# Performance work log

Hardware: AMD Instinct MI355X
Metric: run time of the kernel (lower is better)

## Reference

```python
import jax, jax.numpy as jnp
import numpy as np

N_NODES = 50000
N_EDGES = 800000
D = 96  # d_node = d_edge = hidden = out


def setup_inputs() -> dict:
    key = jax.random.key(0)
    ks = jax.random.split(key, 12)
    s = 1.0 / np.sqrt(D)
    inp = {
        "x": jax.random.normal(ks[0], (N_NODES, D), dtype=jnp.float32),
        "edge_index": jax.random.randint(ks[1], (2, N_EDGES), 0, N_NODES, dtype=jnp.int64),
        "edge_attr": jax.random.normal(ks[2], (N_EDGES, D), dtype=jnp.float32),
        # f_node params: MLP on concat(x, agg_edge_attr) -> [2D] -> D -> D
        "Wn1": jax.random.normal(ks[3], (2 * D, D), dtype=jnp.float32) * s,
        "bn1": jnp.zeros((D,), dtype=jnp.float32),
        "Wn2": jax.random.normal(ks[4], (D, D), dtype=jnp.float32) * s,
        "bn2": jnp.zeros((D,), dtype=jnp.float32),
        # f_edge params: MLP on concat(src, dst, edge_attr) -> [3D] -> D -> D
        "We1": jax.random.normal(ks[5], (3 * D, D), dtype=jnp.float32) * s,
        "be1": jnp.zeros((D,), dtype=jnp.float32),
        "We2": jax.random.normal(ks[6], (D, D), dtype=jnp.float32) * s,
        "be2": jnp.zeros((D,), dtype=jnp.float32),
    }
    return inp


def reference(x, edge_index, edge_attr, Wn1, bn1, Wn2, bn2, We1, be1, We2, be2):
    n_nodes = x.shape[0]
    # f_node: aggregate incoming edge features to destination nodes, then MLP
    agg = jax.ops.segment_sum(edge_attr, edge_index[1], num_segments=n_nodes)  # [N, D]
    hn = jax.nn.relu(jnp.concatenate([x, agg], axis=-1) @ Wn1 + bn1)
    h_v = hn @ Wn2 + bn2  # [N, D]
    # f_edge: gather src/dst node features (x[edge_index[0]], x[edge_index[1]]), then MLP
    src = x[edge_index[0]]  # [E, D]
    dst = x[edge_index[1]]  # [E, D]
    he = jax.nn.relu(jnp.concatenate([src, dst, edge_attr], axis=-1) @ We1 + be1)
    h_e = he @ We2 + be2  # [E, D]
    return (h_v, edge_index, h_e)
```

## Files before the change

### kernel.cpp

```cpp
#include <hip/hip_runtime.h>

#define N_NODES 50000
#define N_EDGES 800000
#define DIM 96

#define BM 64
#define BK 48
#define APAD 52
#define HPAD 100

#define SC_CNT 0
#define SC_OFF 50000
#define SC_CUR 100016
#define SC_BSUM 150016
#define SC_EIDX 150528
#define NBLK_SCAN 196

#define FMA4(C, A, W)        \
  C.x = fmaf(A, W.x, C.x);   \
  C.y = fmaf(A, W.y, C.y);   \
  C.z = fmaf(A, W.z, C.z);   \
  C.w = fmaf(A, W.w, C.w)

#define BIAS_RELU4(C, B)          \
  C.x = fmaxf(C.x + B.x, 0.0f);   \
  C.y = fmaxf(C.y + B.y, 0.0f);   \
  C.z = fmaxf(C.z + B.z, 0.0f);   \
  C.w = fmaxf(C.w + B.w, 0.0f)

#define BIAS4(C, B) \
  C.x += B.x;       \
  C.y += B.y;       \
  C.z += B.z;       \
  C.w += B.w

#define KSTEP(KK, A0, A1)                                                    \
  {                                                                          \
    const float4 w0 =                                                        \
        *reinterpret_cast<const float4*>(&Ws[(k + KK) * DIM + cbase + 0]);   \
    const float4 w1 =                                                        \
        *reinterpret_cast<const float4*>(&Ws[(k + KK) * DIM + cbase + 4]);   \
    const float4 w2 =                                                        \
        *reinterpret_cast<const float4*>(&Ws[(k + KK) * DIM + cbase + 8]);   \
    FMA4(c00, A0, w0);                                                       \
    FMA4(c01, A0, w1);                                                       \
    FMA4(c02, A0, w2);                                                       \
    FMA4(c10, A1, w0);                                                       \
    FMA4(c11, A1, w1);                                                       \
    FMA4(c12, A1, w2);                                                       \
  }

__global__ __launch_bounds__(256) void hist_kernel(const int* __restrict__ ei,
                                                   int* __restrict__ sc) {
  int e = blockIdx.x * 256 + threadIdx.x;
  if (e < N_EDGES) atomicAdd(&sc[SC_CNT + ei[N_EDGES + e]], 1);
}

__global__ __launch_bounds__(256) void scan1_kernel(int* __restrict__ sc) {
  __shared__ int s[256];
  int i = blockIdx.x * 256 + threadIdx.x;
  s[threadIdx.x] = (i < N_NODES) ? sc[SC_CNT + i] : 0;
  __syncthreads();
  for (int off = 128; off > 0; off >>= 1) {
    if (threadIdx.x < off) s[threadIdx.x] += s[threadIdx.x + off];
    __syncthreads();
  }
  if (threadIdx.x == 0) sc[SC_BSUM + blockIdx.x] = s[0];
}

__global__ __launch_bounds__(256) void scan2_kernel(int* __restrict__ sc) {
  __shared__ int s[2][256];
  const int t = threadIdx.x;
  const int v = (t < NBLK_SCAN) ? sc[SC_BSUM + t] : 0;
  int cur = 0;
  s[0][t] = v;
  __syncthreads();
  for (int off = 1; off < 256; off <<= 1) {
    int nv = s[cur][t];
    if (t >= off) nv += s[cur][t - off];
    s[cur ^ 1][t] = nv;
    cur ^= 1;
    __syncthreads();
  }
  if (t < NBLK_SCAN) sc[SC_BSUM + t] = s[cur][t] - v;
}

__global__ __launch_bounds__(256) void scan3_kernel(int* __restrict__ sc) {
  __shared__ int s[2][256];
  const int t = threadIdx.x;
  const int i = blockIdx.x * 256 + t;
  const int v = (i < N_NODES) ? sc[SC_CNT + i] : 0;
  int cur = 0;
  s[0][t] = v;
  __syncthreads();
  for (int off = 1; off < 256; off <<= 1) {
    int nv = s[cur][t];
    if (t >= off) nv += s[cur][t - off];
    s[cur ^ 1][t] = nv;
    cur ^= 1;
    __syncthreads();
  }
  if (i < N_NODES) {
    const int excl = sc[SC_BSUM + blockIdx.x] + s[cur][t] - v;
    sc[SC_OFF + i] = excl;
    sc[SC_CUR + i] = excl;
  }
  if (i == 0) sc[SC_OFF + N_NODES] = N_EDGES;
}

__global__ __launch_bounds__(256) void fill_kernel(const int* __restrict__ ei,
                                                   int* __restrict__ sc) {
  int e = blockIdx.x * 256 + threadIdx.x;
  if (e < N_EDGES) {
    const int d = ei[N_EDGES + e];
    const int pos = atomicAdd(&sc[SC_CUR + d], 1);
    sc[SC_EIDX + pos] = e;
  }
}

__global__ __launch_bounds__(192) void gather_kernel(
    const float* __restrict__ ea, const int* __restrict__ sc,
    float* __restrict__ agg) {
  const int t = threadIdx.x;
  const int ln = t / 24;
  const int q = t - ln * 24;
  const int n = blockIdx.x * 8 + ln;
  const int beg = sc[SC_OFF + n];
  const int end = sc[SC_OFF + n + 1];
  float4 acc = make_float4(0.f, 0.f, 0.f, 0.f);
  int e = (beg < end) ? sc[SC_EIDX + beg] : 0;
  for (int i = beg; i < end; ++i) {
    const int en = (i + 1 < end) ? sc[SC_EIDX + i + 1] : 0;
    const float4 v =
        *reinterpret_cast<const float4*>(ea + (size_t)e * DIM + q * 4);
    acc.x += v.x;
    acc.y += v.y;
    acc.z += v.z;
    acc.w += v.w;
    e = en;
  }
  *reinterpret_cast<float4*>(agg + (size_t)n * DIM + q * 4) = acc;
}

__global__ __launch_bounds__(256) void copy_ei_kernel(
    const int* __restrict__ ei, float* __restrict__ out) {
  int tid = blockIdx.x * 256 + threadIdx.x;
  if (tid < 2 * N_EDGES) out[tid] = (float)ei[tid];
}

__global__ __launch_bounds__(256, 3) void node_mlp_kernel(
    const float* __restrict__ x, const float* __restrict__ agg,
    const float* __restrict__ W1, const float* __restrict__ b1,
    const float* __restrict__ W2, const float* __restrict__ b2,
    float* __restrict__ out) {
  __shared__ float Ws[BK * DIM];
  __shared__ float AH[BM * HPAD];

  const int t = threadIdx.x;
  const int tx = t & 7;
  const int ty = t >> 3;
  const int r0 = ty * 2;
  const int n0 = blockIdx.x * BM;
  const int cbase = tx * 12;

  float4 c00 = make_float4(0.f, 0.f, 0.f, 0.f);
  float4 c01 = c00, c02 = c00, c10 = c00, c11 = c00, c12 = c00;

  for (int ch = 0; ch < 4; ++ch) {
    const int k0 = ch * BK;
    __syncthreads();
#pragma unroll
    for (int m = 0; m < 3; ++m) {
      const int idx = m * 256 + t;
      const int row = idx / 12;
      const int c4 = (idx - row * 12) * 4;
      const int col = k0 + c4;
      int n = n0 + row;
      n = (n < N_NODES) ? n : 0;
      const float* src = (col < DIM) ? x + (size_t)n * DIM + col
                                     : agg + (size_t)n * DIM + (col - DIM);
      *reinterpret_cast<float4*>(&AH[row * APAD + c4]) =
          *reinterpret_cast<const float4*>(src);
    }
#pragma unroll
    for (int m = 0; m < 5; ++m) {
      const int idx = m * 256 + t;
      if (idx < (BK * DIM) / 4) {
        const int wr = idx / 24;
        const int wc = (idx - wr * 24) * 4;
        *reinterpret_cast<float4*>(&Ws[wr * DIM + wc]) =
            *reinterpret_cast<const float4*>(W1 + (size_t)(k0 + wr) * DIM + wc);
      }
    }
    __syncthreads();
#pragma unroll
    for (int k = 0; k < BK; k += 4) {
      const float4 a0v =
          *reinterpret_cast<const float4*>(&AH[(r0 + 0) * APAD + k]);
      const float4 a1v =
          *reinterpret_cast<const float4*>(&AH[(r0 + 1) * APAD + k]);
      KSTEP(0, a0v.x, a1v.x);
      KSTEP(1, a0v.y, a1v.y);
      KSTEP(2, a0v.z, a1v.z);
      KSTEP(3, a0v.w, a1v.w);
    }
  }

  __syncthreads();

  {
    const float4 bb0 = *reinterpret_cast<const float4*>(b1 + cbase + 0);
    const float4 bb1 = *reinterpret_cast<const float4*>(b1 + cbase + 4);
    const float4 bb2 = *reinterpret_cast<const float4*>(b1 + cbase + 8);
    BIAS_RELU4(c00, bb0);
    BIAS_RELU4(c01, bb1);
    BIAS_RELU4(c02, bb2);
    BIAS_RELU4(c10, bb0);
    BIAS_RELU4(c11, bb1);
    BIAS_RELU4(c12, bb2);
    *reinterpret_cast<float4*>(&AH[(r0 + 0) * HPAD + cbase + 0]) = c00;
    *reinterpret_cast<float4*>(&AH[(r0 + 0) * HPAD + cbase + 4]) = c01;
    *reinterpret_cast<float4*>(&AH[(r0 + 0) * HPAD + cbase + 8]) = c02;
    *reinterpret_cast<float4*>(&AH[(r0 + 1) * HPAD + cbase + 0]) = c10;
    *reinterpret_cast<float4*>(&AH[(r0 + 1) * HPAD + cbase + 4]) = c11;
    *reinterpret_cast<float4*>(&AH[(r0 + 1) * HPAD + cbase + 8]) = c12;
  }

  c00 = make_float4(0.f, 0.f, 0.f, 0.f);
  c01 = c00;
  c02 = c00;
  c10 = c00;
  c11 = c00;
  c12 = c00;
  for (int ch = 0; ch < 2; ++ch) {
    const int k0 = ch * BK;
    __syncthreads();
#pragma unroll
    for (int m = 0; m < 5; ++m) {
      const int idx = m * 256 + t;
      if (idx < (BK * DIM) / 4) {
        const int wr = idx / 24;
        const int wc = (idx - wr * 24) * 4;
        *reinterpret_cast<float4*>(&Ws[wr * DIM + wc]) =
            *reinterpret_cast<const float4*>(W2 + (size_t)(k0 + wr) * DIM + wc);
      }
    }
    __syncthreads();
#pragma unroll
    for (int k = 0; k < BK; k += 4) {
      const float4 a0v =
          *reinterpret_cast<const float4*>(&AH[(r0 + 0) * HPAD + k0 + k]);
      const float4 a1v =
          *reinterpret_cast<const float4*>(&AH[(r0 + 1) * HPAD + k0 + k]);
      KSTEP(0, a0v.x, a1v.x);
      KSTEP(1, a0v.y, a1v.y);
      KSTEP(2, a0v.z, a1v.z);
      KSTEP(3, a0v.w, a1v.w);
    }
  }

  {
    const float4 bb0 = *reinterpret_cast<const float4*>(b2 + cbase + 0);
    const float4 bb1 = *reinterpret_cast<const float4*>(b2 + cbase + 4);
    const float4 bb2 = *reinterpret_cast<const float4*>(b2 + cbase + 8);
    BIAS4(c00, bb0);
    BIAS4(c01, bb1);
    BIAS4(c02, bb2);
    BIAS4(c10, bb0);
    BIAS4(c11, bb1);
    BIAS4(c12, bb2);
    const int n_r0 = n0 + r0;
    if (n_r0 < N_NODES) {
      float* o = out + (size_t)n_r0 * DIM + cbase;
      *reinterpret_cast<float4*>(o + 0) = c00;
      *reinterpret_cast<float4*>(o + 4) = c01;
      *reinterpret_cast<float4*>(o + 8) = c02;
    }
    if (n_r0 + 1 < N_NODES) {
      float* o = out + (size_t)(n_r0 + 1) * DIM + cbase;
      *reinterpret_cast<float4*>(o + 0) = c10;
      *reinterpret_cast<float4*>(o + 4) = c11;
      *reinterpret_cast<float4*>(o + 8) = c12;
    }
  }
}

__global__ __launch_bounds__(256, 3) void edge_mlp_kernel(
    const float* __restrict__ x, const int* __restrict__ ei,
    const float* __restrict__ ea, const float* __restrict__ W1,
    const float* __restrict__ b1, const float* __restrict__ W2,
    const float* __restrict__ b2, float* __restrict__ out) {
  __shared__ int s_src[BM];
  __shared__ int s_dst[BM];
  __shared__ float Ws[BK * DIM];
  __shared__ float AH[BM * HPAD];

  const int t = threadIdx.x;
  const int tx = t & 7;
  const int ty = t >> 3;
  const int r0 = ty * 2;
  const int e0 = blockIdx.x * BM;
  const int cbase = tx * 12;

  if (t < BM) {
    s_src[t] = ei[e0 + t];
    s_dst[t] = ei[N_EDGES + e0 + t];
  }

  float4 c00 = make_float4(0.f, 0.f, 0.f, 0.f);
  float4 c01 = c00, c02 = c00, c10 = c00, c11 = c00, c12 = c00;

  for (int ch = 0; ch < 6; ++ch) {
    const int k0 = ch * BK;
    __syncthreads();
#pragma unroll
    for (int m = 0; m < 3; ++m) {
      const int idx = m * 256 + t;
      const int row = idx / 12;
      const int c4 = (idx - row * 12) * 4;
      const int col = k0 + c4;
      const float* src;
      if (col < DIM)
        src = x + (size_t)s_src[row] * DIM + col;
      else if (col < 2 * DIM)
        src = x + (size_t)s_dst[row] * DIM + (col - DIM);
      else
        src = ea + (size_t)(e0 + row) * DIM + (col - 2 * DIM);
      *reinterpret_cast<float4*>(&AH[row * APAD + c4]) =
          *reinterpret_cast<const float4*>(src);
    }
#pragma unroll
    for (int m = 0; m < 5; ++m) {
      const int idx = m * 256 + t;
      if (idx < (BK * DIM) / 4) {
        const int wr = idx / 24;
        const int wc = (idx - wr * 24) * 4;
        *reinterpret_cast<float4*>(&Ws[wr * DIM + wc]) =
            *reinterpret_cast<const float4*>(W1 + (size_t)(k0 + wr) * DIM + wc);
      }
    }
    __syncthreads();
#pragma unroll
    for (int k = 0; k < BK; k += 4) {
      const float4 a0v =
          *reinterpret_cast<const float4*>(&AH[(r0 + 0) * APAD + k]);
      const float4 a1v =
          *reinterpret_cast<const float4*>(&AH[(r0 + 1) * APAD + k]);
      KSTEP(0, a0v.x, a1v.x);
      KSTEP(1, a0v.y, a1v.y);
      KSTEP(2, a0v.z, a1v.z);
      KSTEP(3, a0v.w, a1v.w);
    }
  }

  __syncthreads();

  {
    const float4 bb0 = *reinterpret_cast<const float4*>(b1 + cbase + 0);
    const float4 bb1 = *reinterpret_cast<const float4*>(b1 + cbase + 4);
    const float4 bb2 = *reinterpret_cast<const float4*>(b1 + cbase + 8);
    BIAS_RELU4(c00, bb0);
    BIAS_RELU4(c01, bb1);
    BIAS_RELU4(c02, bb2);
    BIAS_RELU4(c10, bb0);
    BIAS_RELU4(c11, bb1);
    BIAS_RELU4(c12, bb2);
    *reinterpret_cast<float4*>(&AH[(r0 + 0) * HPAD + cbase + 0]) = c00;
    *reinterpret_cast<float4*>(&AH[(r0 + 0) * HPAD + cbase + 4]) = c01;
    *reinterpret_cast<float4*>(&AH[(r0 + 0) * HPAD + cbase + 8]) = c02;
    *reinterpret_cast<float4*>(&AH[(r0 + 1) * HPAD + cbase + 0]) = c10;
    *reinterpret_cast<float4*>(&AH[(r0 + 1) * HPAD + cbase + 4]) = c11;
    *reinterpret_cast<float4*>(&AH[(r0 + 1) * HPAD + cbase + 8]) = c12;
  }

  c00 = make_float4(0.f, 0.f, 0.f, 0.f);
  c01 = c00;
  c02 = c00;
  c10 = c00;
  c11 = c00;
  c12 = c00;
  for (int ch = 0; ch < 2; ++ch) {
    const int k0 = ch * BK;
    __syncthreads();
#pragma unroll
    for (int m = 0; m < 5; ++m) {
      const int idx = m * 256 + t;
      if (idx < (BK * DIM) / 4) {
        const int wr = idx / 24;
        const int wc = (idx - wr * 24) * 4;
        *reinterpret_cast<float4*>(&Ws[wr * DIM + wc]) =
            *reinterpret_cast<const float4*>(W2 + (size_t)(k0 + wr) * DIM + wc);
      }
    }
    __syncthreads();
#pragma unroll
    for (int k = 0; k < BK; k += 4) {
      const float4 a0v =
          *reinterpret_cast<const float4*>(&AH[(r0 + 0) * HPAD + k0 + k]);
      const float4 a1v =
          *reinterpret_cast<const float4*>(&AH[(r0 + 1) * HPAD + k0 + k]);
      KSTEP(0, a0v.x, a1v.x);
      KSTEP(1, a0v.y, a1v.y);
      KSTEP(2, a0v.z, a1v.z);
      KSTEP(3, a0v.w, a1v.w);
    }
  }

  {
    const float4 bb0 = *reinterpret_cast<const float4*>(b2 + cbase + 0);
    const float4 bb1 = *reinterpret_cast<const float4*>(b2 + cbase + 4);
    const float4 bb2 = *reinterpret_cast<const float4*>(b2 + cbase + 8);
    BIAS4(c00, bb0);
    BIAS4(c01, bb1);
    BIAS4(c02, bb2);
    BIAS4(c10, bb0);
    BIAS4(c11, bb1);
    BIAS4(c12, bb2);
    float* o0 = out + (size_t)(e0 + r0) * DIM + cbase;
    float* o1 = out + (size_t)(e0 + r0 + 1) * DIM + cbase;
    *reinterpret_cast<float4*>(o0 + 0) = c00;
    *reinterpret_cast<float4*>(o0 + 4) = c01;
    *reinterpret_cast<float4*>(o0 + 8) = c02;
    *reinterpret_cast<float4*>(o1 + 0) = c10;
    *reinterpret_cast<float4*>(o1 + 4) = c11;
    *reinterpret_cast<float4*>(o1 + 8) = c12;
  }
}

extern "C" void kernel_launch(void* const* d_in, const int* in_sizes, int n_in,
                              void* d_out, int out_size, void* d_ws,
                              size_t ws_size, hipStream_t stream) {
  const float* x = (const float*)d_in[0];
  const int* ei = (const int*)d_in[1];
  const float* edge_attr = (const float*)d_in[2];
  const float* Wn1 = (const float*)d_in[3];
  const float* bn1 = (const float*)d_in[4];
  const float* Wn2 = (const float*)d_in[5];
  const float* bn2 = (const float*)d_in[6];
  const float* We1 = (const float*)d_in[7];
  const float* be1 = (const float*)d_in[8];
  const float* We2 = (const float*)d_in[9];
  const float* be2 = (const float*)d_in[10];

  float* out = (float*)d_out;
  float* agg = (float*)d_ws;

  float* out_hv = out;
  float* out_ei = out + (size_t)N_NODES * DIM;
  float* out_he = out + (size_t)N_NODES * DIM + 2 * (size_t)N_EDGES;

  int* sc = (int*)out_he;

  hipMemsetAsync(sc + SC_CNT, 0, N_NODES * sizeof(int), stream);
  hist_kernel<<<(N_EDGES + 255) / 256, 256, 0, stream>>>(ei, sc);
  scan1_kernel<<<NBLK_SCAN, 256, 0, stream>>>(sc);
  scan2_kernel<<<1, 256, 0, stream>>>(sc);
  scan3_kernel<<<NBLK_SCAN, 256, 0, stream>>>(sc);
  fill_kernel<<<(N_EDGES + 255) / 256, 256, 0, stream>>>(ei, sc);
  gather_kernel<<<N_NODES / 8, 192, 0, stream>>>(edge_attr, sc, agg);

  copy_ei_kernel<<<(2 * N_EDGES + 255) / 256, 256, 0, stream>>>(ei, out_ei);
  node_mlp_kernel<<<(N_NODES + BM - 1) / BM, 256, 0, stream>>>(
      x, agg, Wn1, bn1, Wn2, bn2, out_hv);
  edge_mlp_kernel<<<N_EDGES / BM, 256, 0, stream>>>(x, ei, edge_attr, We1, be1,
                                                    We2, be2, out_he);
}
```

Measured before the change: 1.649 ms.

## Double the MLP row tile and prefetch next K-chunk into registers

Both node and edge MLP kernels move from 64 to 128 rows per block, with each thread now computing 4 rows by 12 columns. This doubles register-level reuse of each weight float4 loaded from shared memory. A register-staged software pipeline is added that loads the next A/W chunk from global memory while the current chunk is computed. W2's first chunk is prefetched during the last layer-1 chunk. The cost is higher register pressure and occupancy lowered to 2 blocks per SM via launch bounds.

```diff
diff --git a/kernel.cpp b/kernel.cpp
--- a/kernel.cpp
+++ b/kernel.cpp
@@ -4,7 +4,7 @@
 #define N_EDGES 800000
 #define DIM 96
 
-#define BM 64
+#define BM 128
 #define BK 48
 #define APAD 52
 #define HPAD 100
@@ -34,7 +34,7 @@
   C.z += B.z;       \
   C.w += B.w
 
-#define KSTEP(KK, A0, A1)                                                    \
+#define KQ(KK, A0, A1, A2, A3)                                               \
   {                                                                          \
     const float4 w0 =                                                        \
         *reinterpret_cast<const float4*>(&Ws[(k + KK) * DIM + cbase + 0]);   \
@@ -42,13 +42,33 @@
         *reinterpret_cast<const float4*>(&Ws[(k + KK) * DIM + cbase + 4]);   \
     const float4 w2 =                                                        \
         *reinterpret_cast<const float4*>(&Ws[(k + KK) * DIM + cbase + 8]);   \
-    FMA4(c00, A0, w0);                                                       \
-    FMA4(c01, A0, w1);                                                       \
-    FMA4(c02, A0, w2);                                                       \
-    FMA4(c10, A1, w0);                                                       \
-    FMA4(c11, A1, w1);                                                       \
-    FMA4(c12, A1, w2);                                                       \
-  }
+    FMA4(c00, A0, w0); FMA4(c01, A0, w1); FMA4(c02, A0, w2);                 \
+    FMA4(c10, A1, w0); FMA4(c11, A1, w1); FMA4(c12, A1, w2);                 \
+    FMA4(c20, A2, w0); FMA4(c21, A2, w1); FMA4(c22, A2, w2);                 \
+    FMA4(c30, A3, w0); FMA4(c31, A3, w1); FMA4(c32, A3, w2);                 \
+  }
+
+#define COMPUTE_CHUNK(STRIDE, KOFF)                                          \
+  _Pragma("unroll") for (int k = 0; k < BK; k += 4) {                        \
+    const float4 av0 = *reinterpret_cast<const float4*>(                     \
+        &AH[(r0 + 0) * STRIDE + KOFF + k]);                                  \
+    const float4 av1 = *reinterpret_cast<const float4*>(                     \
+        &AH[(r0 + 1) * STRIDE + KOFF + k]);                                  \
+    const float4 av2 = *reinterpret_cast<const float4*>(                     \
+        &AH[(r0 + 2) * STRIDE + KOFF + k]);                                  \
+    const float4 av3 = *reinterpret_cast<const float4*>(                     \
+        &AH[(r0 + 3) * STRIDE + KOFF + k]);                                  \
+    KQ(0, av0.x, av1.x, av2.x, av3.x);                                       \
+    KQ(1, av0.y, av1.y, av2.y, av3.y);                                       \
+    KQ(2, av0.z, av1.z, av2.z, av3.z);                                       \
+    KQ(3, av0.w, av1.w, av2.w, av3.w);                                       \
+  }
+
+#define ZERO_ACC()                                          \
+  c00 = make_float4(0.f, 0.f, 0.f, 0.f);                    \
+  c01 = c00; c02 = c00; c10 = c00; c11 = c00; c12 = c00;    \
+  c20 = c00; c21 = c00; c22 = c00; c30 = c00; c31 = c00;    \
+  c32 = c00;
 
 __global__ __launch_bounds__(256) void hist_kernel(const int* __restrict__ ei,
                                                    int* __restrict__ sc) {
@@ -148,7 +168,7 @@
   if (tid < 2 * N_EDGES) out[tid] = (float)ei[tid];
 }
 
-__global__ __launch_bounds__(256, 3) void node_mlp_kernel(
+__global__ __launch_bounds__(256, 2) void node_mlp_kernel(
     const float* __restrict__ x, const float* __restrict__ agg,
     const float* __restrict__ W1, const float* __restrict__ b1,
     const float* __restrict__ W2, const float* __restrict__ b2,
@@ -159,133 +179,144 @@
   const int t = threadIdx.x;
   const int tx = t & 7;
   const int ty = t >> 3;
-  const int r0 = ty * 2;
+  const int r0 = ty * 4;
   const int n0 = blockIdx.x * BM;
   const int cbase = tx * 12;
 
-  float4 c00 = make_float4(0.f, 0.f, 0.f, 0.f);
-  float4 c01 = c00, c02 = c00, c10 = c00, c11 = c00, c12 = c00;
-
+  int arow[6], acol[6];
+#pragma unroll
+  for (int m = 0; m < 6; ++m) {
+    const int idx = m * 256 + t;
+    arow[m] = idx / 12;
+    acol[m] = (idx - arow[m] * 12) * 4;
+  }
+  int wr[5], wc[5];
+#pragma unroll
+  for (int m = 0; m < 5; ++m) {
+    const int idx = m * 256 + t;
+    wr[m] = idx / 24;
+    wc[m] = (idx - wr[m] * 24) * 4;
+  }
+
+  float4 ra[6], rw[5];
+
+  auto load_a = [&](int ch) {
+#pragma unroll
+    for (int m = 0; m < 6; ++m) {
+      const int col = ch * BK + acol[m];
+      int n = n0 + arow[m];
+      n = (n < N_NODES) ? n : 0;
+      const float* p = (col < DIM) ? x + (size_t)n * DIM + col
+                                   : agg + (size_t)n * DIM + (col - DIM);
+      ra[m] = *reinterpret_cast<const float4*>(p);
+    }
+  };
+  auto load_w = [&](const float* W, int ch) {
+#pragma unroll
+    for (int m = 0; m < 5; ++m)
+      if (m < 4 || t < 128)
+        rw[m] = *reinterpret_cast<const float4*>(
+            W + (size_t)(ch * BK + wr[m]) * DIM + wc[m]);
+  };
+  auto store_a = [&]() {
+#pragma unroll
+    for (int m = 0; m < 6; ++m)
+      *reinterpret_cast<float4*>(&AH[arow[m] * APAD + acol[m]]) = ra[m];
+  };
+  auto store_w = [&]() {
+#pragma unroll
+    for (int m = 0; m < 5; ++m)
+      if (m < 4 || t < 128)
+        *reinterpret_cast<float4*>(&Ws[wr[m] * DIM + wc[m]]) = rw[m];
+  };
+
+  float4 c00, c01, c02, c10, c11, c12, c20, c21, c22, c30, c31, c32;
+  ZERO_ACC();
+
+  load_a(0);
+  load_w(W1, 0);
   for (int ch = 0; ch < 4; ++ch) {
-    const int k0 = ch * BK;
-    __syncthreads();
-#pragma unroll
-    for (int m = 0; m < 3; ++m) {
-      const int idx = m * 256 + t;
-      const int row = idx / 12;
-      const int c4 = (idx - row * 12) * 4;
-      const int col = k0 + c4;
-      int n = n0 + row;
-      n = (n < N_NODES) ? n : 0;
-      const float* src = (col < DIM) ? x + (size_t)n * DIM + col
-                                     : agg + (size_t)n * DIM + (col - DIM);
-      *reinterpret_cast<float4*>(&AH[row * APAD + c4]) =
-          *reinterpret_cast<const float4*>(src);
-    }
-#pragma unroll
-    for (int m = 0; m < 5; ++m) {
-      const int idx = m * 256 + t;
-      if (idx < (BK * DIM) / 4) {
-        const int wr = idx / 24;
-        const int wc = (idx - wr * 24) * 4;
-        *reinterpret_cast<float4*>(&Ws[wr * DIM + wc]) =
-            *reinterpret_cast<const float4*>(W1 + (size_t)(k0 + wr) * DIM + wc);
-      }
-    }
-    __syncthreads();
-#pragma unroll
-    for (int k = 0; k < BK; k += 4) {
-      const float4 a0v =
-          *reinterpret_cast<const float4*>(&AH[(r0 + 0) * APAD + k]);
-      const float4 a1v =
-          *reinterpret_cast<const float4*>(&AH[(r0 + 1) * APAD + k]);
-      KSTEP(0, a0v.x, a1v.x);
-      KSTEP(1, a0v.y, a1v.y);
-      KSTEP(2, a0v.z, a1v.z);
-      KSTEP(3, a0v.w, a1v.w);
-    }
-  }
-
-  __syncthreads();
+    store_a();
+    store_w();
+    __syncthreads();
+    if (ch < 3) {
+      load_a(ch + 1);
+      load_w(W1, ch + 1);
+    } else {
+      load_w(W2, 0);
+    }
+    COMPUTE_CHUNK(APAD, 0);
+    __syncthreads();
+  }
 
   {
     const float4 bb0 = *reinterpret_cast<const float4*>(b1 + cbase + 0);
     const float4 bb1 = *reinterpret_cast<const float4*>(b1 + cbase + 4);
     const float4 bb2 = *reinterpret_cast<const float4*>(b1 + cbase + 8);
-    BIAS_RELU4(c00, bb0);
-    BIAS_RELU4(c01, bb1);
-    BIAS_RELU4(c02, bb2);
-    BIAS_RELU4(c10, bb0);
-    BIAS_RELU4(c11, bb1);
-    BIAS_RELU4(c12, bb2);
+    BIAS_RELU4(c00, bb0); BIAS_RELU4(c01, bb1); BIAS_RELU4(c02, bb2);
+    BIAS_RELU4(c10, bb0); BIAS_RELU4(c11, bb1); BIAS_RELU4(c12, bb2);
+    BIAS_RELU4(c20, bb0); BIAS_RELU4(c21, bb1); BIAS_RELU4(c22, bb2);
+    BIAS_RELU4(c30, bb0); BIAS_RELU4(c31, bb1); BIAS_RELU4(c32, bb2);
     *reinterpret_cast<float4*>(&AH[(r0 + 0) * HPAD + cbase + 0]) = c00;
     *reinterpret_cast<float4*>(&AH[(r0 + 0) * HPAD + cbase + 4]) = c01;
     *reinterpret_cast<float4*>(&AH[(r0 + 0) * HPAD + cbase + 8]) = c02;
     *reinterpret_cast<float4*>(&AH[(r0 + 1) * HPAD + cbase + 0]) = c10;
     *reinterpret_cast<float4*>(&AH[(r0 + 1) * HPAD + cbase + 4]) = c11;
     *reinterpret_cast<float4*>(&AH[(r0 + 1) * HPAD + cbase + 8]) = c12;
-  }
-
-  c00 = make_float4(0.f, 0.f, 0.f, 0.f);
-  c01 = c00;
-  c02 = c00;
-  c10 = c00;
-  c11 = c00;
-  c12 = c00;
-  for (int ch = 0; ch < 2; ++ch) {
-    const int k0 = ch * BK;
-    __syncthreads();
-#pragma unroll
-    for (int m = 0; m < 5; ++m) {
-      const int idx = m * 256 + t;
-      if (idx < (BK * DIM) / 4) {
-        const int wr = idx / 24;
-        const int wc = (idx - wr * 24) * 4;
-        *reinterpret_cast<float4*>(&Ws[wr * DIM + wc]) =
-            *reinterpret_cast<const float4*>(W2 + (size_t)(k0 + wr) * DIM + wc);
-      }
-    }
-    __syncthreads();
-#pragma unroll
-    for (int k = 0; k < BK; k += 4) {
-      const float4 a0v =
-          *reinterpret_cast<const float4*>(&AH[(r0 + 0) * HPAD + k0 + k]);
-      const float4 a1v =
-          *reinterpret_cast<const float4*>(&AH[(r0 + 1) * HPAD + k0 + k]);
-      KSTEP(0, a0v.x, a1v.x);
-      KSTEP(1, a0v.y, a1v.y);
-      KSTEP(2, a0v.z, a1v.z);
-      KSTEP(3, a0v.w, a1v.w);
-    }
-  }
+    *reinterpret_cast<float4*>(&AH[(r0 + 2) * HPAD + cbase + 0]) = c20;
+    *reinterpret_cast<float4*>(&AH[(r0 + 2) * HPAD + cbase + 4]) = c21;
+    *reinterpret_cast<float4*>(&AH[(r0 + 2) * HPAD + cbase + 8]) = c22;
+    *reinterpret_cast<float4*>(&AH[(r0 + 3) * HPAD + cbase + 0]) = c30;
+    *reinterpret_cast<float4*>(&AH[(r0 + 3) * HPAD + cbase + 4]) = c31;
+    *reinterpret_cast<float4*>(&AH[(r0 + 3) * HPAD + cbase + 8]) = c32;
+  }
+  store_w();
+  __syncthreads();
+
+  load_w(W2, 1);
+  ZERO_ACC();
+  COMPUTE_CHUNK(HPAD, 0);
+  __syncthreads();
+  store_w();
+  __syncthreads();
+  COMPUTE_CHUNK(HPAD, BK);
 
   {
     const float4 bb0 = *reinterpret_cast<const float4*>(b2 + cbase + 0);
     const float4 bb1 = *reinterpret_cast<const float4*>(b2 + cbase + 4);
     const float4 bb2 = *reinterpret_cast<const float4*>(b2 + cbase + 8);
-    BIAS4(c00, bb0);
-    BIAS4(c01, bb1);
-    BIAS4(c02, bb2);
-    BIAS4(c10, bb0);
-    BIAS4(c11, bb1);
-    BIAS4(c12, bb2);
-    const int n_r0 = n0 + r0;
-    if (n_r0 < N_NODES) {
-      float* o = out + (size_t)n_r0 * DIM + cbase;
+    BIAS4(c00, bb0); BIAS4(c01, bb1); BIAS4(c02, bb2);
+    BIAS4(c10, bb0); BIAS4(c11, bb1); BIAS4(c12, bb2);
+    BIAS4(c20, bb0); BIAS4(c21, bb1); BIAS4(c22, bb2);
+    BIAS4(c30, bb0); BIAS4(c31, bb1); BIAS4(c32, bb2);
+    if (n0 + r0 + 0 < N_NODES) {
+      float* o = out + (size_t)(n0 + r0 + 0) * DIM + cbase;
       *reinterpret_cast<float4*>(o + 0) = c00;
       *reinterpret_cast<float4*>(o + 4) = c01;
       *reinterpret_cast<float4*>(o + 8) = c02;
     }
-    if (n_r0 + 1 < N_NODES) {
-      float* o = out + (size_t)(n_r0 + 1) * DIM + cbase;
+    if (n0 + r0 + 1 < N_NODES) {
+      float* o = out + (size_t)(n0 + r0 + 1) * DIM + cbase;
       *reinterpret_cast<float4*>(o + 0) = c10;
       *reinterpret_cast<float4*>(o + 4) = c11;
       *reinterpret_cast<float4*>(o + 8) = c12;
     }
-  }
-}
-
-__global__ __launch_bounds__(256, 3) void edge_mlp_kernel(
+    if (n0 + r0 + 2 < N_NODES) {
+      float* o = out + (size_t)(n0 + r0 + 2) * DIM + cbase;
+      *reinterpret_cast<float4*>(o + 0) = c20;
+      *reinterpret_cast<float4*>(o + 4) = c21;
+      *reinterpret_cast<float4*>(o + 8) = c22;
+    }
+    if (n0 + r0 + 3 < N_NODES) {
+      float* o = out + (size_t)(n0 + r0 + 3) * DIM + cbase;
+      *reinterpret_cast<float4*>(o + 0) = c30;
+      *reinterpret_cast<float4*>(o + 4) = c31;
+      *reinterpret_cast<float4*>(o + 8) = c32;
+    }
+  }
+}
+
+__global__ __launch_bounds__(256, 2) void edge_mlp_kernel(
     const float* __restrict__ x, const int* __restrict__ ei,
     const float* __restrict__ ea, const float* __restrict__ W1,
     const float* __restrict__ b1, const float* __restrict__ W2,
@@ -298,132 +329,142 @@
   const int t = threadIdx.x;
   const int tx = t & 7;
   const int ty = t >> 3;
-  const int r0 = ty * 2;
+  const int r0 = ty * 4;
   const int e0 = blockIdx.x * BM;
   const int cbase = tx * 12;
 
-  if (t < BM) {
+  int arow[6], acol[6];
+#pragma unroll
+  for (int m = 0; m < 6; ++m) {
+    const int idx = m * 256 + t;
+    arow[m] = idx / 12;
+    acol[m] = (idx - arow[m] * 12) * 4;
+  }
+  int wr[5], wc[5];
+#pragma unroll
+  for (int m = 0; m < 5; ++m) {
+    const int idx = m * 256 + t;
+    wr[m] = idx / 24;
+    wc[m] = (idx - wr[m] * 24) * 4;
+  }
+
+  if (t < BM)
     s_src[t] = ei[e0 + t];
-    s_dst[t] = ei[N_EDGES + e0 + t];
-  }
-
-  float4 c00 = make_float4(0.f, 0.f, 0.f, 0.f);
-  float4 c01 = c00, c02 = c00, c10 = c00, c11 = c00, c12 = c00;
-
+  else
+    s_dst[t - BM] = ei[N_EDGES + e0 + (t - BM)];
+  __syncthreads();
+
+  float4 ra[6], rw[5];
+
+  auto load_a = [&](int ch) {
+#pragma unroll
+    for (int m = 0; m < 6; ++m) {
+      const int col = ch * BK + acol[m];
+      const int row = arow[m];
+      const float* p;
+      if (col < DIM)
+        p = x + (size_t)s_src[row] * DIM + col;
+      else if (col < 2 * DIM)
+        p = x + (size_t)s_dst[row] * DIM + (col - DIM);
+      else
+        p = ea + (size_t)(e0 + row) * DIM + (col - 2 * DIM);
+      ra[m] = *reinterpret_cast<const float4*>(p);
+    }
+  };
+  auto load_w = [&](const float* W, int ch) {
+#pragma unroll
+    for (int m = 0; m < 5; ++m)
+      if (m < 4 || t < 128)
+        rw[m] = *reinterpret_cast<const float4*>(
+            W + (size_t)(ch * BK + wr[m]) * DIM + wc[m]);
+  };
+  auto store_a = [&]() {
+#pragma unroll
+    for (int m = 0; m < 6; ++m)
+      *reinterpret_cast<float4*>(&AH[arow[m] * APAD + acol[m]]) = ra[m];
+  };
+  auto store_w = [&]() {
+#pragma unroll
+    for (int m = 0; m < 5; ++m)
+      if (m < 4 || t < 128)
+        *reinterpret_cast<float4*>(&Ws[wr[m] * DIM + wc[m]]) = rw[m];
+  };
+
+  float4 c00, c01, c02, c10, c11, c12, c20, c21, c22, c30, c31, c32;
+  ZERO_ACC();
+
+  load_a(0);
+  load_w(W1, 0);
   for (int ch = 0; ch < 6; ++ch) {
-    const int k0 = ch * BK;
-    __syncthreads();
-#pragma unroll
-    for (int m = 0; m < 3; ++m) {
-      const int idx = m * 256 + t;
-      const int row = idx / 12;
-      const int c4 = (idx - row * 12) * 4;
-      const int col = k0 + c4;
-      const float* src;
-      if (col < DIM)
-        src = x + (size_t)s_src[row] * DIM + col;
-      else if (col < 2 * DIM)
-        src = x + (size_t)s_dst[row] * DIM + (col - DIM);
-      else
-        src = ea + (size_t)(e0 + row) * DIM + (col - 2 * DIM);
-      *reinterpret_cast<float4*>(&AH[row * APAD + c4]) =
-          *reinterpret_cast<const float4*>(src);
-    }
-#pragma unroll
-    for (int m = 0; m < 5; ++m) {
-      const int idx = m * 256 + t;
-      if (idx < (BK * DIM) / 4) {
-        const int wr = idx / 24;
-        const int wc = (idx - wr * 24) * 4;
-        *reinterpret_cast<float4*>(&Ws[wr * DIM + wc]) =
-            *reinterpret_cast<const float4*>(W1 + (size_t)(k0 + wr) * DIM + wc);
-      }
-    }
-    __syncthreads();
-#pragma unroll
-    for (int k = 0; k < BK; k += 4) {
-      const float4 a0v =
-          *reinterpret_cast<const float4*>(&AH[(r0 + 0) * APAD + k]);
-      const float4 a1v =
-          *reinterpret_cast<const float4*>(&AH[(r0 + 1) * APAD + k]);
-      KSTEP(0, a0v.x, a1v.x);
-      KSTEP(1, a0v.y, a1v.y);
-      KSTEP(2, a0v.z, a1v.z);
-      KSTEP(3, a0v.w, a1v.w);
-    }
-  }
-
-  __syncthreads();
+    store_a();
+    store_w();
+    __syncthreads();
+    if (ch < 5) {
+      load_a(ch + 1);
+      load_w(W1, ch + 1);
+    } else {
+      load_w(W2, 0);
+    }
+    COMPUTE_CHUNK(APAD, 0);
+    __syncthreads();
+  }
 
   {
     const float4 bb0 = *reinterpret_cast<const float4*>(b1 + cbase + 0);
     const float4 bb1 = *reinterpret_cast<const float4*>(b1 + cbase + 4);
     const float4 bb2 = *reinterpret_cast<const float4*>(b1 + cbase + 8);
-    BIAS_RELU4(c00, bb0);
-    BIAS_RELU4(c01, bb1);
-    BIAS_RELU4(c02, bb2);
-    BIAS_RELU4(c10, bb0);
-    BIAS_RELU4(c11, bb1);
-    BIAS_RELU4(c12, bb2);
+    BIAS_RELU4(c00, bb0); BIAS_RELU4(c01, bb1); BIAS_RELU4(c02, bb2);
+    BIAS_RELU4(c10, bb0); BIAS_RELU4(c11, bb1); BIAS_RELU4(c12, bb2);
+    BIAS_RELU4(c20, bb0); BIAS_RELU4(c21, bb1); BIAS_RELU4(c22, bb2);
+    BIAS_RELU4(c30, bb0); BIAS_RELU4(c31, bb1); BIAS_RELU4(c32, bb2);
     *reinterpret_cast<float4*>(&AH[(r0 + 0) * HPAD + cbase + 0]) = c00;
     *reinterpret_cast<float4*>(&AH[(r0 + 0) * HPAD + cbase + 4]) = c01;
     *reinterpret_cast<float4*>(&AH[(r0 + 0) * HPAD + cbase + 8]) = c02;
     *reinterpret_cast<float4*>(&AH[(r0 + 1) * HPAD + cbase + 0]) = c10;
     *reinterpret_cast<float4*>(&AH[(r0 + 1) * HPAD + cbase + 4]) = c11;
     *reinterpret_cast<float4*>(&AH[(r0 + 1) * HPAD + cbase + 8]) = c12;
-  }
-
-  c00 = make_float4(0.f, 0.f, 0.f, 0.f);
-  c01 = c00;
-  c02 = c00;
-  c10 = c00;
-  c11 = c00;
-  c12 = c00;
-  for (int ch = 0; ch < 2; ++ch) {
-    const int k0 = ch * BK;
-    __syncthreads();
-#pragma unroll
-    for (int m = 0; m < 5; ++m) {
-      const int idx = m * 256 + t;
-      if (idx < (BK * DIM) / 4) {
-        const int wr = idx / 24;
-        const int wc = (idx - wr * 24) * 4;
-        *reinterpret_cast<float4*>(&Ws[wr * DIM + wc]) =
-            *reinterpret_cast<const float4*>(W2 + (size_t)(k0 + wr) * DIM + wc);
-      }
-    }
-    __syncthreads();
-#pragma unroll
-    for (int k = 0; k < BK; k += 4) {
-      const float4 a0v =
-          *reinterpret_cast<const float4*>(&AH[(r0 + 0) * HPAD + k0 + k]);
-      const float4 a1v =
-          *reinterpret_cast<const float4*>(&AH[(r0 + 1) * HPAD + k0 + k]);
-      KSTEP(0, a0v.x, a1v.x);
-      KSTEP(1, a0v.y, a1v.y);
-      KSTEP(2, a0v.z, a1v.z);
-      KSTEP(3, a0v.w, a1v.w);
-    }
-  }
+    *reinterpret_cast<float4*>(&AH[(r0 + 2) * HPAD + cbase + 0]) = c20;
+    *reinterpret_cast<float4*>(&AH[(r0 + 2) * HPAD + cbase + 4]) = c21;
+    *reinterpret_cast<float4*>(&AH[(r0 + 2) * HPAD + cbase + 8]) = c22;
+    *reinterpret_cast<float4*>(&AH[(r0 + 3) * HPAD + cbase + 0]) = c30;
+    *reinterpret_cast<float4*>(&AH[(r0 + 3) * HPAD + cbase + 4]) = c31;
+    *reinterpret_cast<float4*>(&AH[(r0 + 3) * HPAD + cbase + 8]) = c32;
+  }
+  store_w();
+  __syncthreads();
+
+  load_w(W2, 1);
+  ZERO_ACC();
+  COMPUTE_CHUNK(HPAD, 0);
+  __syncthreads();
+  store_w();
+  __syncthreads();
+  COMPUTE_CHUNK(HPAD, BK);
 
   {
     const float4 bb0 = *reinterpret_cast<const float4*>(b2 + cbase + 0);
     const float4 bb1 = *reinterpret_cast<const float4*>(b2 + cbase + 4);
     const float4 bb2 = *reinterpret_cast<const float4*>(b2 + cbase + 8);
-    BIAS4(c00, bb0);
-    BIAS4(c01, bb1);
-    BIAS4(c02, bb2);
-    BIAS4(c10, bb0);
-    BIAS4(c11, bb1);
-    BIAS4(c12, bb2);
-    float* o0 = out + (size_t)(e0 + r0) * DIM + cbase;
+    BIAS4(c00, bb0); BIAS4(c01, bb1); BIAS4(c02, bb2);
+    BIAS4(c10, bb0); BIAS4(c11, bb1); BIAS4(c12, bb2);
+    BIAS4(c20, bb0); BIAS4(c21, bb1); BIAS4(c22, bb2);
+    BIAS4(c30, bb0); BIAS4(c31, bb1); BIAS4(c32, bb2);
+    float* o0 = out + (size_t)(e0 + r0 + 0) * DIM + cbase;
     float* o1 = out + (size_t)(e0 + r0 + 1) * DIM + cbase;
+    float* o2 = out + (size_t)(e0 + r0 + 2) * DIM + cbase;
+    float* o3 = out + (size_t)(e0 + r0 + 3) * DIM + cbase;
     *reinterpret_cast<float4*>(o0 + 0) = c00;
     *reinterpret_cast<float4*>(o0 + 4) = c01;
     *reinterpret_cast<float4*>(o0 + 8) = c02;
     *reinterpret_cast<float4*>(o1 + 0) = c10;
     *reinterpret_cast<float4*>(o1 + 4) = c11;
     *reinterpret_cast<float4*>(o1 + 8) = c12;
+    *reinterpret_cast<float4*>(o2 + 0) = c20;
+    *reinterpret_cast<float4*>(o2 + 4) = c21;
+    *reinterpret_cast<float4*>(o2 + 8) = c22;
+    *reinterpret_cast<float4*>(o3 + 0) = c30;
+    *reinterpret_cast<float4*>(o3 + 4) = c31;
+    *reinterpret_cast<float4*>(o3 + 8) = c32;
   }
 }
 
```

After: 5.965 ms. 3.62x slower.
